# Optimization experiments

Hardware: AMD Instinct MI355X
Metric: run time of the kernel (lower is better)

The kernel has to match this reference:

```python
import jax, jax.numpy as jnp
import numpy as np

KSIZE = 8
STRIDE = 4
HEADS = 8
DIM_HEAD = 32
EPS = 1e-5


def _layernorm(x, g, b):
    m = jnp.mean(x, axis=-1, keepdims=True)
    v = jnp.mean(jnp.square(x - m), axis=-1, keepdims=True)
    return (x - m) / jnp.sqrt(v + EPS) * g + b


def setup_inputs() -> dict:
    key = jax.random.key(0)
    ks = jax.random.split(key, 4)
    B, H, W, C = 8, 64, 64, 256
    inner = HEADS * DIM_HEAD  # 256
    x = jax.random.normal(ks[0], (B, H, W, C), dtype=jnp.float32)
    return {
        "x": x,
        "ln1_g": jnp.ones((C,), jnp.float32),
        "ln1_b": jnp.zeros((C,), jnp.float32),
        "ln2_g": jnp.ones((C,), jnp.float32),
        "ln2_b": jnp.zeros((C,), jnp.float32),
        "w_qkv": jax.random.normal(ks[1], (C, inner * 3), jnp.float32) * 0.02,
        "w_out": jax.random.normal(ks[2], (inner, C), jnp.float32) * 0.02,
        "b_out": jnp.zeros((C,), jnp.float32),
    }


def reference(x, ln1_g, ln1_b, ln2_g, ln2_b, w_qkv, w_out, b_out):
    B, H, W, C = x.shape
    k, s = KSIZE, STRIDE
    nH = (H - k) // s + 1
    nW = (W - k) // s + 1
    L = nH * nW
    n = k * k  # tokens per window

    # window index grids (im2col / unfold)
    rows = jnp.arange(nH)[:, None] * s + jnp.arange(k)[None, :]  # [nH, k]
    cols = jnp.arange(nW)[:, None] * s + jnp.arange(k)[None, :]  # [nW, k]
    ridx = rows[:, None, :, None]  # [nH,1,k,1]
    cidx = cols[None, :, None, :]  # [1,nW,1,k]

    # unfold: [B, nH, nW, k, k, C] -> [(B L), (k k), C]
    patches = x[:, ridx, cidx, :].reshape(B * L, n, C)

    # LocalAttention2D.norm then AttentionBlock.norm
    p = _layernorm(patches, ln1_g, ln1_b)
    h = _layernorm(p, ln2_g, ln2_b)

    qkv = h @ w_qkv  # [(B L), n, 3*inner]
    q, kk, v = jnp.split(qkv, 3, axis=-1)
    q = q.reshape(B * L, n, HEADS, DIM_HEAD)
    kk = kk.reshape(B * L, n, HEADS, DIM_HEAD)
    v = v.reshape(B * L, n, HEADS, DIM_HEAD)

    scale = DIM_HEAD ** -0.5
    dots = jnp.einsum('bnhd,bmhd->bhnm', q, kk) * scale
    attn = jax.nn.softmax(dots, axis=-1)
    o = jnp.einsum('bhnm,bmhd->bnhd', attn, v).reshape(B * L, n, HEADS * DIM_HEAD)
    o = o @ w_out + b_out  # [(B L), n, C]

    # fold (col2im overlap-add)
    o = o.reshape(B, nH, nW, k, k, C)
    out = jnp.zeros((B, H, W, C), x.dtype).at[:, ridx, cidx, :].add(o)

    # normalization: fold(unfold(ones)) == overlap counts
    counts = jnp.zeros((H, W), x.dtype).at[ridx, cidx].add(1.0)
    return out / counts[None, :, :, None]
```

## Files before the change

kernel.cpp:

```cpp
#include <hip/hip_runtime.h>
#include <hip/hip_bf16.h>
#include <cstdint>
#include <cstddef>

#define LN_EPS 1e-5f
#define B_    8
#define HW_   64
#define C_    256
#define NTOK  (B_ * HW_ * HW_)
#define HEADS_ 8
#define DH_    32

__global__ __launch_bounds__(256) void ln_stats_kernel(
    const float* __restrict__ x, const float* __restrict__ g1,
    const float* __restrict__ b1, float4* __restrict__ stats)
{
    const int gid  = blockIdx.x * 256 + threadIdx.x;
    const int tok  = gid >> 6;
    const int lane = gid & 63;
    if (tok >= NTOK) return;
    const float4 xv = reinterpret_cast<const float4*>(x + (size_t)tok * C_)[lane];
    float s  = xv.x + xv.y + xv.z + xv.w;
    float sq = xv.x*xv.x + xv.y*xv.y + xv.z*xv.z + xv.w*xv.w;
    for (int off = 32; off; off >>= 1) {
        s  += __shfl_xor(s, off);
        sq += __shfl_xor(sq, off);
    }
    const float m1 = s * (1.0f / 256.0f);
    const float r1 = rsqrtf(fmaxf(sq * (1.0f / 256.0f) - m1 * m1, 0.0f) + LN_EPS);
    const float4 g = reinterpret_cast<const float4*>(g1)[lane];
    const float4 b = reinterpret_cast<const float4*>(b1)[lane];
    const float y0 = (xv.x - m1) * r1 * g.x + b.x;
    const float y1 = (xv.y - m1) * r1 * g.y + b.y;
    const float y2 = (xv.z - m1) * r1 * g.z + b.z;
    const float y3 = (xv.w - m1) * r1 * g.w + b.w;
    float s2  = y0 + y1 + y2 + y3;
    float sq2 = y0*y0 + y1*y1 + y2*y2 + y3*y3;
    for (int off = 32; off; off >>= 1) {
        s2  += __shfl_xor(s2, off);
        sq2 += __shfl_xor(sq2, off);
    }
    const float m2 = s2 * (1.0f / 256.0f);
    const float r2 = rsqrtf(fmaxf(sq2 * (1.0f / 256.0f) - m2 * m2, 0.0f) + LN_EPS);
    if (lane == 0) stats[tok] = make_float4(m1, r1, m2, r2);
}

__global__ __launch_bounds__(256) void qkv_kernel(
    const float* __restrict__ x, const float4* __restrict__ stats,
    const float* __restrict__ g1, const float* __restrict__ b1,
    const float* __restrict__ g2, const float* __restrict__ b2,
    const float* __restrict__ w, float* __restrict__ qkv)
{
    __shared__ float At[16][72];
    __shared__ float Bt[16][64];
    const int tid  = threadIdx.x;
    const int tok0 = blockIdx.y * 64;
    const int n0   = blockIdx.x * 64;
    const int ty = tid >> 4, tx = tid & 15;
    const int st = tid >> 2, sseg = tid & 3;
    const int bk = tid >> 4, bx = tid & 15;
    const float4 s4 = stats[tok0 + st];
    const float* xrow = x + (size_t)(tok0 + st) * C_;
    float acc[4][4] = {};
    for (int kk = 0; kk < 16; ++kk) {
        const int k0 = kk * 16;
        const int ka = k0 + sseg * 4;
        const float4 xv  = *reinterpret_cast<const float4*>(xrow + ka);
        const float4 g1v = *reinterpret_cast<const float4*>(g1 + ka);
        const float4 b1v = *reinterpret_cast<const float4*>(b1 + ka);
        const float4 g2v = *reinterpret_cast<const float4*>(g2 + ka);
        const float4 b2v = *reinterpret_cast<const float4*>(b2 + ka);
        const float h0 = ((xv.x - s4.x)*s4.y*g1v.x + b1v.x - s4.z)*s4.w*g2v.x + b2v.x;
        const float h1 = ((xv.y - s4.x)*s4.y*g1v.y + b1v.y - s4.z)*s4.w*g2v.y + b2v.y;
        const float h2 = ((xv.z - s4.x)*s4.y*g1v.z + b1v.z - s4.z)*s4.w*g2v.z + b2v.z;
        const float h3 = ((xv.w - s4.x)*s4.y*g1v.w + b1v.w - s4.z)*s4.w*g2v.w + b2v.w;
        const float4 wv = *reinterpret_cast<const float4*>(w + (size_t)(k0 + bk) * 768 + n0 + bx * 4);
        __syncthreads();
        At[sseg*4+0][st] = h0;
        At[sseg*4+1][st] = h1;
        At[sseg*4+2][st] = h2;
        At[sseg*4+3][st] = h3;
        *reinterpret_cast<float4*>(&Bt[bk][bx*4]) = wv;
        __syncthreads();
        #pragma unroll
        for (int k = 0; k < 16; ++k) {
            const float4 a = *reinterpret_cast<const float4*>(&At[k][ty*4]);
            const float4 b = *reinterpret_cast<const float4*>(&Bt[k][tx*4]);
            acc[0][0] += a.x*b.x; acc[0][1] += a.x*b.y; acc[0][2] += a.x*b.z; acc[0][3] += a.x*b.w;
            acc[1][0] += a.y*b.x; acc[1][1] += a.y*b.y; acc[1][2] += a.y*b.z; acc[1][3] += a.y*b.w;
            acc[2][0] += a.z*b.x; acc[2][1] += a.z*b.y; acc[2][2] += a.z*b.z; acc[2][3] += a.z*b.w;
            acc[3][0] += a.w*b.x; acc[3][1] += a.w*b.y; acc[3][2] += a.w*b.z; acc[3][3] += a.w*b.w;
        }
    }
    #pragma unroll
    for (int r = 0; r < 4; ++r) {
        const float4 o = make_float4(acc[r][0], acc[r][1], acc[r][2], acc[r][3]);
        *reinterpret_cast<float4*>(qkv + (size_t)(tok0 + ty*4 + r) * 768 + n0 + tx*4) = o;
    }
}

__global__ __launch_bounds__(256) void attn_kernel(
    const float* __restrict__ qkv, float* __restrict__ out,
    int gi, int gj, int nJ, int do_store)
{
    __shared__ float q_lds[64][36];
    __shared__ float kT[32][68];
    __shared__ float v_lds[64][36];
    __shared__ float p_lds[64][68];
    const int tid = threadIdx.x;
    const int b  = blockIdx.y;
    const int hd = blockIdx.z;
    const int pi = 2 * (blockIdx.x / nJ) + gi;
    const int pj = 2 * (blockIdx.x % nJ) + gj;
    const int t = tid >> 2, seg = tid & 3;
    const int pr = t >> 3, pc = t & 7;
    const size_t pixbase = ((size_t)((b * 64 + 4*pi + pr) * 64) + (4*pj + pc));
    {
        const size_t base = pixbase * 768 + hd * 32 + seg * 8;
        const float4 qa = *reinterpret_cast<const float4*>(qkv + base);
        const float4 qb = *reinterpret_cast<const float4*>(qkv + base + 4);
        const float4 ka = *reinterpret_cast<const float4*>(qkv + base + 256);
        const float4 kb = *reinterpret_cast<const float4*>(qkv + base + 260);
        const float4 va = *reinterpret_cast<const float4*>(qkv + base + 512);
        const float4 vb = *reinterpret_cast<const float4*>(qkv + base + 516);
        *reinterpret_cast<float4*>(&q_lds[t][seg*8    ]) = qa;
        *reinterpret_cast<float4*>(&q_lds[t][seg*8 + 4]) = qb;
        *reinterpret_cast<float4*>(&v_lds[t][seg*8    ]) = va;
        *reinterpret_cast<float4*>(&v_lds[t][seg*8 + 4]) = vb;
        const int d0 = seg * 8;
        kT[d0+0][t] = ka.x; kT[d0+1][t] = ka.y; kT[d0+2][t] = ka.z; kT[d0+3][t] = ka.w;
        kT[d0+4][t] = kb.x; kT[d0+5][t] = kb.y; kT[d0+6][t] = kb.z; kT[d0+7][t] = kb.w;
    }
    __syncthreads();
    const float scale = 0.17677669529663687f;
    const int tr = tid >> 4, tc = tid & 15;
    float s[4][4] = {};
    #pragma unroll
    for (int kk = 0; kk < 4; ++kk) {
        float qreg[4][8];
        #pragma unroll
        for (int i = 0; i < 4; ++i) {
            const float4 qv0 = *reinterpret_cast<const float4*>(&q_lds[tr*4 + i][kk*8]);
            const float4 qv1 = *reinterpret_cast<const float4*>(&q_lds[tr*4 + i][kk*8 + 4]);
            qreg[i][0] = qv0.x; qreg[i][1] = qv0.y; qreg[i][2] = qv0.z; qreg[i][3] = qv0.w;
            qreg[i][4] = qv1.x; qreg[i][5] = qv1.y; qreg[i][6] = qv1.z; qreg[i][7] = qv1.w;
        }
        #pragma unroll
        for (int w = 0; w < 8; ++w) {
            const float4 kv = *reinterpret_cast<const float4*>(&kT[kk*8 + w][tc*4]);
            const float ka[4] = {kv.x, kv.y, kv.z, kv.w};
            #pragma unroll
            for (int i = 0; i < 4; ++i) {
                #pragma unroll
                for (int j = 0; j < 4; ++j)
                    s[i][j] = fmaf(qreg[i][w], ka[j], s[i][j]);
            }
        }
    }
    float mrow[4], sum[4];
    #pragma unroll
    for (int i = 0; i < 4; ++i) {
        s[i][0] *= scale; s[i][1] *= scale; s[i][2] *= scale; s[i][3] *= scale;
        mrow[i] = fmaxf(fmaxf(s[i][0], s[i][1]), fmaxf(s[i][2], s[i][3]));
    }
    #pragma unroll
    for (int off = 1; off < 16; off <<= 1)
        #pragma unroll
        for (int i = 0; i < 4; ++i)
            mrow[i] = fmaxf(mrow[i], __shfl_xor(mrow[i], off));
    #pragma unroll
    for (int i = 0; i < 4; ++i) {
        sum[i] = 0.f;
        #pragma unroll
        for (int j = 0; j < 4; ++j) {
            s[i][j] = __expf(s[i][j] - mrow[i]);
            sum[i] += s[i][j];
        }
    }
    #pragma unroll
    for (int off = 1; off < 16; off <<= 1)
        #pragma unroll
        for (int i = 0; i < 4; ++i)
            sum[i] += __shfl_xor(sum[i], off);
    #pragma unroll
    for (int i = 0; i < 4; ++i) {
        const float rs = 1.0f / sum[i];
        #pragma unroll
        for (int j = 0; j < 4; ++j)
            p_lds[tr*4 + i][tc*4 + j] = s[i][j] * rs;
    }
    __syncthreads();
    float4 o0 = make_float4(0,0,0,0), o1 = make_float4(0,0,0,0);
    for (int jc = 0; jc < 64; ++jc) {
        const float a = p_lds[t][jc];
        const float4 v0 = *reinterpret_cast<const float4*>(&v_lds[jc][seg*8]);
        const float4 v1 = *reinterpret_cast<const float4*>(&v_lds[jc][seg*8 + 4]);
        o0.x = fmaf(a, v0.x, o0.x); o0.y = fmaf(a, v0.y, o0.y);
        o0.z = fmaf(a, v0.z, o0.z); o0.w = fmaf(a, v0.w, o0.w);
        o1.x = fmaf(a, v1.x, o1.x); o1.y = fmaf(a, v1.y, o1.y);
        o1.z = fmaf(a, v1.z, o1.z); o1.w = fmaf(a, v1.w, o1.w);
    }
    float* op = out + pixbase * 256 + hd * 32 + seg * 8;
    if (do_store) {
        *reinterpret_cast<float4*>(op)     = o0;
        *reinterpret_cast<float4*>(op + 4) = o1;
    } else {
        float4 c0 = *reinterpret_cast<const float4*>(op);
        float4 c1 = *reinterpret_cast<const float4*>(op + 4);
        c0.x += o0.x; c0.y += o0.y; c0.z += o0.z; c0.w += o0.w;
        c1.x += o1.x; c1.y += o1.y; c1.z += o1.z; c1.w += o1.w;
        *reinterpret_cast<float4*>(op)     = c0;
        *reinterpret_cast<float4*>(op + 4) = c1;
    }
}

__global__ __launch_bounds__(256) void proj_kernel(
    float* __restrict__ out, const float* __restrict__ w, const float* __restrict__ bo)
{
    __shared__ float At[16][36];
    __shared__ float Bt[16][256];
    const int tid  = threadIdx.x;
    const int tok0 = blockIdx.x * 32;
    const int ty = tid >> 5, tx = tid & 31;
    const int st = tid >> 2, sseg = tid & 3;
    const int bc = (tid & 63) * 4, bkb = tid >> 6;
    float ascale = 0.f;
    if (tid < 128) {
        const int token = tok0 + st;
        const int hp = (token >> 6) & 63, wp = token & 63;
        const float cnt = ((hp >= 4 && hp < 60) ? 2.f : 1.f) * ((wp >= 4 && wp < 60) ? 2.f : 1.f);
        ascale = 1.0f / cnt;
    }
    float acc[4][8] = {};
    for (int kk = 0; kk < 16; ++kk) {
        const int k0 = kk * 16;
        float4 av = make_float4(0,0,0,0);
        if (tid < 128)
            av = *reinterpret_cast<const float4*>(out + (size_t)(tok0 + st) * 256 + k0 + sseg * 4);
        float4 wv[4];
        #pragma unroll
        for (int u = 0; u < 4; ++u)
            wv[u] = *reinterpret_cast<const float4*>(w + (size_t)(k0 + bkb*4 + u) * 256 + bc);
        __syncthreads();
        if (tid < 128) {
            At[sseg*4+0][st] = av.x * ascale;
            At[sseg*4+1][st] = av.y * ascale;
            At[sseg*4+2][st] = av.z * ascale;
            At[sseg*4+3][st] = av.w * ascale;
        }
        #pragma unroll
        for (int u = 0; u < 4; ++u)
            *reinterpret_cast<float4*>(&Bt[bkb*4+u][bc]) = wv[u];
        __syncthreads();
        #pragma unroll
        for (int k = 0; k < 16; ++k) {
            const float4 a  = *reinterpret_cast<const float4*>(&At[k][ty*4]);
            const float4 b0 = *reinterpret_cast<const float4*>(&Bt[k][tx*4]);
            const float4 b1 = *reinterpret_cast<const float4*>(&Bt[k][128 + tx*4]);
            acc[0][0] += a.x*b0.x; acc[0][1] += a.x*b0.y; acc[0][2] += a.x*b0.z; acc[0][3] += a.x*b0.w;
            acc[0][4] += a.x*b1.x; acc[0][5] += a.x*b1.y; acc[0][6] += a.x*b1.z; acc[0][7] += a.x*b1.w;
            acc[1][0] += a.y*b0.x; acc[1][1] += a.y*b0.y; acc[1][2] += a.y*b0.z; acc[1][3] += a.y*b0.w;
            acc[1][4] += a.y*b1.x; acc[1][5] += a.y*b1.y; acc[1][6] += a.y*b1.z; acc[1][7] += a.y*b1.w;
            acc[2][0] += a.z*b0.x; acc[2][1] += a.z*b0.y; acc[2][2] += a.z*b0.z; acc[2][3] += a.z*b0.w;
            acc[2][4] += a.z*b1.x; acc[2][5] += a.z*b1.y; acc[2][6] += a.z*b1.z; acc[2][7] += a.z*b1.w;
            acc[3][0] += a.w*b0.x; acc[3][1] += a.w*b0.y; acc[3][2] += a.w*b0.z; acc[3][3] += a.w*b0.w;
            acc[3][4] += a.w*b1.x; acc[3][5] += a.w*b1.y; acc[3][6] += a.w*b1.z; acc[3][7] += a.w*b1.w;
        }
    }
    const float4 bo0 = *reinterpret_cast<const float4*>(bo + tx*4);
    const float4 bo1 = *reinterpret_cast<const float4*>(bo + 128 + tx*4);
    #pragma unroll
    for (int r = 0; r < 4; ++r) {
        float* orow = out + (size_t)(tok0 + ty*4 + r) * 256;
        const float4 o0 = make_float4(acc[r][0]+bo0.x, acc[r][1]+bo0.y, acc[r][2]+bo0.z, acc[r][3]+bo0.w);
        const float4 o1 = make_float4(acc[r][4]+bo1.x, acc[r][5]+bo1.y, acc[r][6]+bo1.z, acc[r][7]+bo1.w);
        *reinterpret_cast<float4*>(orow + tx*4)       = o0;
        *reinterpret_cast<float4*>(orow + 128 + tx*4) = o1;
    }
}

extern "C" void kernel_launch(void* const* d_in, const int* in_sizes, int n_in,
                              void* d_out, int out_size, void* d_ws, size_t ws_size,
                              hipStream_t stream)
{
    const float* x     = (const float*)d_in[0];
    const float* ln1_g = (const float*)d_in[1];
    const float* ln1_b = (const float*)d_in[2];
    const float* ln2_g = (const float*)d_in[3];
    const float* ln2_b = (const float*)d_in[4];
    const float* w_qkv = (const float*)d_in[5];
    const float* w_out = (const float*)d_in[6];
    const float* b_out = (const float*)d_in[7];
    float* out = (float*)d_out;
    float* ws  = (float*)d_ws;

    float4* stats = (float4*)ws;
    float*  qkv   = ws + (size_t)NTOK * 4;

    ln_stats_kernel<<<NTOK / 4, 256, 0, stream>>>(x, ln1_g, ln1_b, stats);
    qkv_kernel<<<dim3(12, NTOK / 64), 256, 0, stream>>>(
        x, stats, ln1_g, ln1_b, ln2_g, ln2_b, w_qkv, qkv);
    for (int g = 0; g < 4; ++g) {
        const int gi = g >> 1, gj = g & 1;
        const int nI = gi ? 7 : 8, nJ = gj ? 7 : 8;
        attn_kernel<<<dim3(nI * nJ, B_, HEADS_), 256, 0, stream>>>(
            qkv, out, gi, gj, nJ, (g == 0) ? 1 : 0);
    }
    proj_kernel<<<NTOK / 32, 256, 0, stream>>>(out, w_out, b_out);
}
```

Measured before the change: 459.6 us.

## Write per-window attention outputs to buffer and fold them inside projection GEMM

```diff
diff --git a/kernel.cpp b/kernel.cpp
--- a/kernel.cpp
+++ b/kernel.cpp
@@ -10,6 +10,7 @@
 #define NTOK  (B_ * HW_ * HW_)
 #define HEADS_ 8
 #define DH_    32
+#define NPATCH 15
 
 __global__ __launch_bounds__(256) void ln_stats_kernel(
     const float* __restrict__ x, const float* __restrict__ g1,
@@ -99,6 +100,195 @@
     }
 }
 
+__global__ __launch_bounds__(256) void attn_o_kernel(
+    const float* __restrict__ qkv, float* __restrict__ obuf)
+{
+    __shared__ float q_lds[64][36];
+    __shared__ float kT[32][68];
+    __shared__ float v_lds[64][36];
+    __shared__ float p_lds[64][68];
+    const int tid = threadIdx.x;
+    const int b  = blockIdx.y;
+    const int hd = blockIdx.z;
+    const int pi = blockIdx.x / NPATCH;
+    const int pj = blockIdx.x % NPATCH;
+    const int t = tid >> 2, seg = tid & 3;
+    const int pr = t >> 3, pc = t & 7;
+    const size_t pixbase = ((size_t)((b * 64 + 4*pi + pr) * 64) + (4*pj + pc));
+    {
+        const size_t base = pixbase * 768 + hd * 32 + seg * 8;
+        const float4 qa = *reinterpret_cast<const float4*>(qkv + base);
+        const float4 qb = *reinterpret_cast<const float4*>(qkv + base + 4);
+        const float4 ka = *reinterpret_cast<const float4*>(qkv + base + 256);
+        const float4 kb = *reinterpret_cast<const float4*>(qkv + base + 260);
+        const float4 va = *reinterpret_cast<const float4*>(qkv + base + 512);
+        const float4 vb = *reinterpret_cast<const float4*>(qkv + base + 516);
+        *reinterpret_cast<float4*>(&q_lds[t][seg*8    ]) = qa;
+        *reinterpret_cast<float4*>(&q_lds[t][seg*8 + 4]) = qb;
+        *reinterpret_cast<float4*>(&v_lds[t][seg*8    ]) = va;
+        *reinterpret_cast<float4*>(&v_lds[t][seg*8 + 4]) = vb;
+        const int d0 = seg * 8;
+        kT[d0+0][t] = ka.x; kT[d0+1][t] = ka.y; kT[d0+2][t] = ka.z; kT[d0+3][t] = ka.w;
+        kT[d0+4][t] = kb.x; kT[d0+5][t] = kb.y; kT[d0+6][t] = kb.z; kT[d0+7][t] = kb.w;
+    }
+    __syncthreads();
+    const float scale = 0.17677669529663687f;
+    const int tr = tid >> 4, tc = tid & 15;
+    float s[4][4] = {};
+    #pragma unroll
+    for (int kk = 0; kk < 4; ++kk) {
+        float qreg[4][8];
+        #pragma unroll
+        for (int i = 0; i < 4; ++i) {
+            const float4 qv0 = *reinterpret_cast<const float4*>(&q_lds[tr*4 + i][kk*8]);
+            const float4 qv1 = *reinterpret_cast<const float4*>(&q_lds[tr*4 + i][kk*8 + 4]);
+            qreg[i][0] = qv0.x; qreg[i][1] = qv0.y; qreg[i][2] = qv0.z; qreg[i][3] = qv0.w;
+            qreg[i][4] = qv1.x; qreg[i][5] = qv1.y; qreg[i][6] = qv1.z; qreg[i][7] = qv1.w;
+        }
+        #pragma unroll
+        for (int w = 0; w < 8; ++w) {
+            const float4 kv = *reinterpret_cast<const float4*>(&kT[kk*8 + w][tc*4]);
+            const float ka[4] = {kv.x, kv.y, kv.z, kv.w};
+            #pragma unroll
+            for (int i = 0; i < 4; ++i) {
+                #pragma unroll
+                for (int j = 0; j < 4; ++j)
+                    s[i][j] = fmaf(qreg[i][w], ka[j], s[i][j]);
+            }
+        }
+    }
+    float mrow[4], sum[4];
+    #pragma unroll
+    for (int i = 0; i < 4; ++i) {
+        s[i][0] *= scale; s[i][1] *= scale; s[i][2] *= scale; s[i][3] *= scale;
+        mrow[i] = fmaxf(fmaxf(s[i][0], s[i][1]), fmaxf(s[i][2], s[i][3]));
+    }
+    #pragma unroll
+    for (int off = 1; off < 16; off <<= 1)
+        #pragma unroll
+        for (int i = 0; i < 4; ++i)
+            mrow[i] = fmaxf(mrow[i], __shfl_xor(mrow[i], off));
+    #pragma unroll
+    for (int i = 0; i < 4; ++i) {
+        sum[i] = 0.f;
+        #pragma unroll
+        for (int j = 0; j < 4; ++j) {
+            s[i][j] = __expf(s[i][j] - mrow[i]);
+            sum[i] += s[i][j];
+        }
+    }
+    #pragma unroll
+    for (int off = 1; off < 16; off <<= 1)
+        #pragma unroll
+        for (int i = 0; i < 4; ++i)
+            sum[i] += __shfl_xor(sum[i], off);
+    #pragma unroll
+    for (int i = 0; i < 4; ++i) {
+        const float rs = 1.0f / sum[i];
+        #pragma unroll
+        for (int j = 0; j < 4; ++j)
+            p_lds[tr*4 + i][tc*4 + j] = s[i][j] * rs;
+    }
+    __syncthreads();
+    float4 o0 = make_float4(0,0,0,0), o1 = make_float4(0,0,0,0);
+    for (int jc = 0; jc < 64; ++jc) {
+        const float a = p_lds[t][jc];
+        const float4 v0 = *reinterpret_cast<const float4*>(&v_lds[jc][seg*8]);
+        const float4 v1 = *reinterpret_cast<const float4*>(&v_lds[jc][seg*8 + 4]);
+        o0.x = fmaf(a, v0.x, o0.x); o0.y = fmaf(a, v0.y, o0.y);
+        o0.z = fmaf(a, v0.z, o0.z); o0.w = fmaf(a, v0.w, o0.w);
+        o1.x = fmaf(a, v1.x, o1.x); o1.y = fmaf(a, v1.y, o1.y);
+        o1.z = fmaf(a, v1.z, o1.z); o1.w = fmaf(a, v1.w, o1.w);
+    }
+    float* op = obuf + ((size_t)(b * 225 + pi * NPATCH + pj) * 64 + t) * 256 + hd * 32 + seg * 8;
+    *reinterpret_cast<float4*>(op)     = o0;
+    *reinterpret_cast<float4*>(op + 4) = o1;
+}
+
+__global__ __launch_bounds__(256) void proj_gather_kernel(
+    const float* __restrict__ obuf, const float* __restrict__ w,
+    const float* __restrict__ bo, float* __restrict__ out)
+{
+    __shared__ float At[16][36];
+    __shared__ float Bt[16][256];
+    const int tid  = threadIdx.x;
+    const int tok0 = blockIdx.x * 32;
+    const int ty = tid >> 5, tx = tid & 31;
+    const int st = tid >> 2, sseg = tid & 3;
+    const int bc = (tid & 63) * 4, bkb = tid >> 6;
+    const float* s00 = obuf; const float* s01 = obuf;
+    const float* s10 = obuf; const float* s11 = obuf;
+    if (tid < 128) {
+        const int token = tok0 + st;
+        const int bb = token >> 12;
+        const int hp = (token >> 6) & 63, wp = token & 63;
+        const int pil = (hp >= 4) ? ((hp - 4) >> 2) : 0;
+        const int pih = (hp >> 2) > 14 ? 14 : (hp >> 2);
+        const int pjl = (wp >= 4) ? ((wp - 4) >> 2) : 0;
+        const int pjh = (wp >> 2) > 14 ? 14 : (wp >> 2);
+        const size_t base_b = (size_t)bb * 225;
+        s00 = obuf + ((base_b + pil * NPATCH + pjl) * 64 + (8*(hp-4*pil) + (wp-4*pjl))) * 256;
+        s01 = obuf + ((base_b + pil * NPATCH + pjh) * 64 + (8*(hp-4*pil) + (wp-4*pjh))) * 256;
+        s10 = obuf + ((base_b + pih * NPATCH + pjl) * 64 + (8*(hp-4*pih) + (wp-4*pjl))) * 256;
+        s11 = obuf + ((base_b + pih * NPATCH + pjh) * 64 + (8*(hp-4*pih) + (wp-4*pjh))) * 256;
+    }
+    float acc[4][8] = {};
+    for (int kk = 0; kk < 16; ++kk) {
+        const int k0 = kk * 16;
+        float4 av = make_float4(0,0,0,0);
+        if (tid < 128) {
+            const int off = k0 + sseg * 4;
+            const float4 v0 = *reinterpret_cast<const float4*>(s00 + off);
+            const float4 v1 = *reinterpret_cast<const float4*>(s01 + off);
+            const float4 v2 = *reinterpret_cast<const float4*>(s10 + off);
+            const float4 v3 = *reinterpret_cast<const float4*>(s11 + off);
+            av.x = ((v0.x + v1.x) + (v2.x + v3.x)) * 0.25f;
+            av.y = ((v0.y + v1.y) + (v2.y + v3.y)) * 0.25f;
+            av.z = ((v0.z + v1.z) + (v2.z + v3.z)) * 0.25f;
+            av.w = ((v0.w + v1.w) + (v2.w + v3.w)) * 0.25f;
+        }
+        float4 wv[4];
+        #pragma unroll
+        for (int u = 0; u < 4; ++u)
+            wv[u] = *reinterpret_cast<const float4*>(w + (size_t)(k0 + bkb*4 + u) * 256 + bc);
+        __syncthreads();
+        if (tid < 128) {
+            At[sseg*4+0][st] = av.x;
+            At[sseg*4+1][st] = av.y;
+            At[sseg*4+2][st] = av.z;
+            At[sseg*4+3][st] = av.w;
+        }
+        #pragma unroll
+        for (int u = 0; u < 4; ++u)
+            *reinterpret_cast<float4*>(&Bt[bkb*4+u][bc]) = wv[u];
+        __syncthreads();
+        #pragma unroll
+        for (int k = 0; k < 16; ++k) {
+            const float4 a  = *reinterpret_cast<const float4*>(&At[k][ty*4]);
+            const float4 b0 = *reinterpret_cast<const float4*>(&Bt[k][tx*4]);
+            const float4 b1 = *reinterpret_cast<const float4*>(&Bt[k][128 + tx*4]);
+            acc[0][0] += a.x*b0.x; acc[0][1] += a.x*b0.y; acc[0][2] += a.x*b0.z; acc[0][3] += a.x*b0.w;
+            acc[0][4] += a.x*b1.x; acc[0][5] += a.x*b1.y; acc[0][6] += a.x*b1.z; acc[0][7] += a.x*b1.w;
+            acc[1][0] += a.y*b0.x; acc[1][1] += a.y*b0.y; acc[1][2] += a.y*b0.z; acc[1][3] += a.y*b0.w;
+            acc[1][4] += a.y*b1.x; acc[1][5] += a.y*b1.y; acc[1][6] += a.y*b1.z; acc[1][7] += a.y*b1.w;
+            acc[2][0] += a.z*b0.x; acc[2][1] += a.z*b0.y; acc[2][2] += a.z*b0.z; acc[2][3] += a.z*b0.w;
+            acc[2][4] += a.z*b1.x; acc[2][5] += a.z*b1.y; acc[2][6] += a.z*b1.z; acc[2][7] += a.z*b1.w;
+            acc[3][0] += a.w*b0.x; acc[3][1] += a.w*b0.y; acc[3][2] += a.w*b0.z; acc[3][3] += a.w*b0.w;
+            acc[3][4] += a.w*b1.x; acc[3][5] += a.w*b1.y; acc[3][6] += a.w*b1.z; acc[3][7] += a.w*b1.w;
+        }
+    }
+    const float4 bo0 = *reinterpret_cast<const float4*>(bo + tx*4);
+    const float4 bo1 = *reinterpret_cast<const float4*>(bo + 128 + tx*4);
+    #pragma unroll
+    for (int r = 0; r < 4; ++r) {
+        float* orow = out + (size_t)(tok0 + ty*4 + r) * 256;
+        const float4 o0 = make_float4(acc[r][0]+bo0.x, acc[r][1]+bo0.y, acc[r][2]+bo0.z, acc[r][3]+bo0.w);
+        const float4 o1 = make_float4(acc[r][4]+bo1.x, acc[r][5]+bo1.y, acc[r][6]+bo1.z, acc[r][7]+bo1.w);
+        *reinterpret_cast<float4*>(orow + tx*4)       = o0;
+        *reinterpret_cast<float4*>(orow + 128 + tx*4) = o1;
+    }
+}
+
 __global__ __launch_bounds__(256) void attn_kernel(
     const float* __restrict__ qkv, float* __restrict__ out,
     int gi, int gj, int nJ, int do_store)
@@ -292,19 +482,30 @@
     const float* w_out = (const float*)d_in[6];
     const float* b_out = (const float*)d_in[7];
     float* out = (float*)d_out;
-    float* ws  = (float*)d_ws;
+    char*  ws  = (char*)d_ws;
+
+    const size_t stats_b = (size_t)NTOK * 16;
+    const size_t qkv_b   = (size_t)NTOK * 768 * 4;
+    const size_t obuf_b  = (size_t)B_ * 225 * 64 * 256 * 4;
 
     float4* stats = (float4*)ws;
-    float*  qkv   = ws + (size_t)NTOK * 4;
+    float*  qkv   = (float*)(ws + stats_b);
+    float*  obuf  = (float*)(ws + stats_b + qkv_b);
 
     ln_stats_kernel<<<NTOK / 4, 256, 0, stream>>>(x, ln1_g, ln1_b, stats);
     qkv_kernel<<<dim3(12, NTOK / 64), 256, 0, stream>>>(
         x, stats, ln1_g, ln1_b, ln2_g, ln2_b, w_qkv, qkv);
-    for (int g = 0; g < 4; ++g) {
-        const int gi = g >> 1, gj = g & 1;
-        const int nI = gi ? 7 : 8, nJ = gj ? 7 : 8;
-        attn_kernel<<<dim3(nI * nJ, B_, HEADS_), 256, 0, stream>>>(
-            qkv, out, gi, gj, nJ, (g == 0) ? 1 : 0);
-    }
-    proj_kernel<<<NTOK / 32, 256, 0, stream>>>(out, w_out, b_out);
-}
+
+    if (ws_size >= stats_b + qkv_b + obuf_b) {
+        attn_o_kernel<<<dim3(225, B_, HEADS_), 256, 0, stream>>>(qkv, obuf);
+        proj_gather_kernel<<<NTOK / 32, 256, 0, stream>>>(obuf, w_out, b_out, out);
+    } else {
+        for (int g = 0; g < 4; ++g) {
+            const int gi = g >> 1, gj = g & 1;
+            const int nI = gi ? 7 : 8, nJ = gj ? 7 : 8;
+            attn_kernel<<<dim3(nI * nJ, B_, HEADS_), 256, 0, stream>>>(
+                qkv, out, gi, gj, nJ, (g == 0) ? 1 : 0);
+        }
+        proj_kernel<<<NTOK / 32, 256, 0, stream>>>(out, w_out, b_out);
+    }
+}
```

After: 463.8 us. About the same (+0.9%).
